# Kernel tuning notes

Measured on AMD Instinct MI355X. Metric: run time of the kernel, lower is better.

Reference implementation:

```python
import jax, jax.numpy as jnp
import numpy as np

LAMBDA_CHAMFER = 1.0
LAMBDA_EDGE = 0.1


def setup_inputs() -> dict:
    key = jax.random.key(0)
    k1, k2, k3 = jax.random.split(key, 3)
    B, N, M, E = 8, 4096, 4096, 12288
    pred_vertices = jax.random.normal(k1, (B, N, 3), dtype=jnp.float32)
    gt_vertices = jax.random.normal(k2, (B, M, 3), dtype=jnp.float32)
    edges = jax.random.randint(k3, (E, 2), 0, N, dtype=jnp.int64)
    return {"pred_vertices": pred_vertices, "gt_vertices": gt_vertices, "edges": edges}


def _pairwise_dist(p1, p2):
    # ||x - y|| computed via the expanded form to avoid a [B,N,M,3] intermediate.
    # dist2[b,n,m] = |p1[b,n]|^2 + |p2[b,m]|^2 - 2 * p1[b,n] . p2[b,m]
    sq1 = jnp.sum(p1 * p1, axis=-1)  # [B, N]
    sq2 = jnp.sum(p2 * p2, axis=-1)  # [B, M]
    cross = jnp.einsum('bnd,bmd->bnm', p1, p2)  # [B, N, M]
    dist2 = sq1[:, :, None] + sq2[:, None, :] - 2.0 * cross
    return jnp.sqrt(jnp.maximum(dist2, 0.0))


def chamfer_distance(p1, p2):
    dist = _pairwise_dist(p1, p2)  # [B, N, M]
    min_p1 = jnp.min(dist, axis=2)  # [B, N] nearest gt for each pred point
    min_p2 = jnp.min(dist, axis=1)  # [B, M] nearest pred for each gt point
    return jnp.mean(min_p1) + jnp.mean(min_p2)


def edge_length_regularization(vertices, edges):
    v1 = vertices[:, edges[:, 0]]  # [B, E, 3]
    v2 = vertices[:, edges[:, 1]]  # [B, E, 3]
    lengths = jnp.linalg.norm(v1 - v2, axis=2)  # [B, E]
    return jnp.var(lengths, ddof=1)  # torch.var is unbiased by default


def reference(pred_vertices, gt_vertices, edges):
    cd = chamfer_distance(pred_vertices, gt_vertices)
    edge_loss = edge_length_regularization(pred_vertices, edges)
    return LAMBDA_CHAMFER * cd + LAMBDA_EDGE * edge_loss
```

## Files before the change

### kernel.cpp

```cpp
#include <hip/hip_runtime.h>
#include <hip/hip_bf16.h>
#include <float.h>

constexpr int B = 8, N = 4096, M = 4096, E = 12288;
constexpr int BLOCK = 256;
constexpr int VEC = 4;
constexpr int QPB = BLOCK * VEC;
constexpr int QT = N / QPB;
constexpr int SEG = 8;
constexpr int RPS = M / SEG;
constexpr int CHAM_BLOCKS = 2 * B * QT * SEG;
constexpr int EDGE_BLOCKS = (B * E) / BLOCK;
constexpr int EPB = E / BLOCK;


__global__ __launch_bounds__(BLOCK) void fused_kernel(
    const float* __restrict__ pred, const float* __restrict__ gt,
    const int* __restrict__ edges, unsigned* __restrict__ ws) {
    const int bid = blockIdx.x;
    const int t = threadIdx.x;

    if (bid < CHAM_BLOCKS) {
        const int dir = bid >> 8;
        const int r   = bid & 255;
        const int b   = r >> 5;
        const int rem = r & 31;
        const int qt  = rem >> 3;
        const int sg  = rem & 7;
        const float* __restrict__ q   = dir ? gt   : pred;
        const float* __restrict__ ref = dir ? pred : gt;
        unsigned* __restrict__ minOut = ws + dir * (B * N) + b * N + qt * QPB;

        float qx[VEC], qy[VEC], qz[VEC], h1[VEC];
#pragma unroll
        for (int i = 0; i < VEC; i++) {
            const int n = qt * QPB + i * BLOCK + t;
            const float* p = q + ((size_t)b * N + n) * 3;
            qx[i] = p[0]; qy[i] = p[1]; qz[i] = p[2];
            h1[i] = 0.5f * (qx[i] * qx[i] + qy[i] * qy[i] + qz[i] * qz[i]);
        }

        __shared__ float4 tile[RPS];
        {
            const float2* rb = (const float2*)(ref + ((size_t)b * M + sg * RPS) * 3);
            const float2 r0 = rb[3 * t], r1 = rb[3 * t + 1], r2 = rb[3 * t + 2];
            const float x0 = r0.x, y0 = r0.y, z0 = r1.x;
            const float x1 = r1.y, y1 = r2.x, z1 = r2.y;
            tile[2 * t]     = make_float4(x0, y0, z0, 0.5f * (x0*x0 + y0*y0 + z0*z0));
            tile[2 * t + 1] = make_float4(x1, y1, z1, 0.5f * (x1*x1 + y1*y1 + z1*z1));
        }
        __syncthreads();

        float mn[VEC];
#pragma unroll
        for (int i = 0; i < VEC; i++) mn[i] = FLT_MAX;

#pragma unroll 8
        for (int m = 0; m < RPS; ++m) {
            const float4 p = tile[m];
#pragma unroll
            for (int i = 0; i < VEC; ++i) {
                float d = h1[i] + p.w;
                d = fmaf(-qx[i], p.x, d);
                d = fmaf(-qy[i], p.y, d);
                d = fmaf(-qz[i], p.z, d);
                mn[i] = fminf(mn[i], d);
            }
        }

#pragma unroll
        for (int i = 0; i < VEC; ++i) {
            const unsigned u = __float_as_uint(fmaxf(mn[i], 0.0f));
            atomicMin(minOut + i * BLOCK + t, u);
        }
    } else {
        const int eb = bid - CHAM_BLOCKS;
        const int b  = eb / EPB;
        const int e  = (eb - b * EPB) * BLOCK + t;
        const int i0 = edges[2 * e], i1 = edges[2 * e + 1];
        const float* p0 = pred + ((size_t)b * N + i0) * 3;
        const float* p1 = pred + ((size_t)b * N + i1) * 3;
        const float dx = p0[0] - p1[0];
        const float dy = p0[1] - p1[1];
        const float dz = p0[2] - p1[2];
        float L  = sqrtf(dx * dx + dy * dy + dz * dz);
        float L2 = L * L;
#pragma unroll
        for (int o = 32; o > 0; o >>= 1) {
            L  += __shfl_down(L, o, 64);
            L2 += __shfl_down(L2, o, 64);
        }
        __shared__ float w1[4], w2[4];
        const int wave = t >> 6, lane = t & 63;
        if (lane == 0) { w1[wave] = L; w2[wave] = L2; }
        __syncthreads();
        if (t == 0) {
            float* wsf = (float*)(ws + 2 * B * N);
            wsf[2 * eb]     = w1[0] + w1[1] + w1[2] + w1[3];
            wsf[2 * eb + 1] = w2[0] + w2[1] + w2[2] + w2[3];
        }
    }
}

__global__ __launch_bounds__(1024) void final_kernel(
    const unsigned* __restrict__ ws, float* __restrict__ out) {
    const int t = threadIdx.x;

    float sc = 0.0f;
#pragma unroll 8
    for (int k = 0; k < 64; ++k) {
        const float h = __uint_as_float(ws[t + k * 1024]);
        sc += sqrtf(fmaxf(2.0f * h, 0.0f));
    }
    float s1 = 0.0f, s2 = 0.0f;
    if (t < EDGE_BLOCKS) {
        const float* wsf = (const float*)(ws + 2 * B * N);
        s1 = wsf[2 * t];
        s2 = wsf[2 * t + 1];
    }
#pragma unroll
    for (int o = 32; o > 0; o >>= 1) {
        sc += __shfl_down(sc, o, 64);
        s1 += __shfl_down(s1, o, 64);
        s2 += __shfl_down(s2, o, 64);
    }
    __shared__ float w[3][16];
    const int wave = t >> 6, lane = t & 63;
    if (lane == 0) { w[0][wave] = sc; w[1][wave] = s1; w[2][wave] = s2; }
    __syncthreads();
    if (t == 0) {
        float S = 0.0f, A = 0.0f, C = 0.0f;
#pragma unroll
        for (int i = 0; i < 16; i++) { S += w[0][i]; A += w[1][i]; C += w[2][i]; }
        const float K = (float)(B * E);
        const float var = (C - A * A / K) / (K - 1.0f);
        out[0] = S / 32768.0f + 0.1f * var;
    }
}

extern "C" void kernel_launch(void* const* d_in, const int* in_sizes, int n_in,
                              void* d_out, int out_size, void* d_ws, size_t ws_size,
                              hipStream_t stream) {
    const float* pred  = (const float*)d_in[0];
    const float* gt    = (const float*)d_in[1];
    const int*   edges = (const int*)d_in[2];
    float* out = (float*)d_out;
    unsigned* ws = (unsigned*)d_ws;

    fused_kernel<<<CHAM_BLOCKS + EDGE_BLOCKS, BLOCK, 0, stream>>>(pred, gt, edges, ws);
    final_kernel<<<1, 1024, 0, stream>>>(ws, out);
}
```

Measured before the change: 95.20 us.

## Load full reference set per block and reduce minima in shared memory

Each 1024-thread block now stages the entire 4096-point reference set into shared memory and splits it across 8 thread groups, which then combine their partial minima in shared memory. This replaces the global atomicMin path and the separate sqrt/mean pass over 64K values in the final kernel. Each block also writes a partial sum of distances, so the final kernel only reduces 256 values. In exchange, each block uses 64KB+ of LDS and handles 2 queries per thread instead of 4, which may lower occupancy and register-level reuse. The inner loop is unrolled over 4 reference points with two independent min accumulators.

```diff
diff --git a/kernel.cpp b/kernel.cpp
--- a/kernel.cpp
+++ b/kernel.cpp
@@ -3,80 +3,99 @@
 #include <float.h>
 
 constexpr int B = 8, N = 4096, M = 4096, E = 12288;
-constexpr int BLOCK = 256;
-constexpr int VEC = 4;
-constexpr int QPB = BLOCK * VEC;
-constexpr int QT = N / QPB;
-constexpr int SEG = 8;
-constexpr int RPS = M / SEG;
-constexpr int CHAM_BLOCKS = 2 * B * QT * SEG;
-constexpr int EDGE_BLOCKS = (B * E) / BLOCK;
-constexpr int EPB = E / BLOCK;
+constexpr int CBLOCK = 1024;
+constexpr int CHAM_BLOCKS = 256;
+constexpr int EDGE_BLOCKS = (B * E) / CBLOCK;
+constexpr int SPLIT = 8;
+constexpr int RPT = M / SPLIT;
+constexpr int VEC = 2;
+constexpr int QG = CBLOCK / SPLIT;
 
 
-__global__ __launch_bounds__(BLOCK) void fused_kernel(
+__global__ __launch_bounds__(CBLOCK) void fused_kernel(
     const float* __restrict__ pred, const float* __restrict__ gt,
-    const int* __restrict__ edges, unsigned* __restrict__ ws) {
+    const int* __restrict__ edges, float* __restrict__ ws) {
     const int bid = blockIdx.x;
     const int t = threadIdx.x;
 
+    __shared__ float4 tile[M];
+    __shared__ float red[SPLIT * 256];
+    __shared__ float wsum[16];
+
     if (bid < CHAM_BLOCKS) {
-        const int dir = bid >> 8;
-        const int r   = bid & 255;
-        const int b   = r >> 5;
-        const int rem = r & 31;
-        const int qt  = rem >> 3;
-        const int sg  = rem & 7;
+        const int dir = bid >> 7;
+        const int b   = (bid >> 4) & 7;
+        const int qt  = bid & 15;
         const float* __restrict__ q   = dir ? gt   : pred;
         const float* __restrict__ ref = dir ? pred : gt;
-        unsigned* __restrict__ minOut = ws + dir * (B * N) + b * N + qt * QPB;
 
+        {
+            const float2* rb = (const float2*)(ref + (size_t)b * M * 3) + 6 * t;
+            const float2 r0 = rb[0], r1 = rb[1], r2 = rb[2];
+            const float2 r3 = rb[3], r4 = rb[4], r5 = rb[5];
+            const float x0=r0.x,y0=r0.y,z0=r1.x, x1=r1.y,y1=r2.x,z1=r2.y;
+            const float x2=r3.x,y2=r3.y,z2=r4.x, x3=r4.y,y3=r5.x,z3=r5.y;
+            tile[4*t+0] = make_float4(x0,y0,z0, 0.5f*(x0*x0+y0*y0+z0*z0));
+            tile[4*t+1] = make_float4(x1,y1,z1, 0.5f*(x1*x1+y1*y1+z1*z1));
+            tile[4*t+2] = make_float4(x2,y2,z2, 0.5f*(x2*x2+y2*y2+z2*z2));
+            tile[4*t+3] = make_float4(x3,y3,z3, 0.5f*(x3*x3+y3*y3+z3*z3));
+        }
+
+        const int qloc = t & (QG - 1);
+        const int s    = t >> 7;
         float qx[VEC], qy[VEC], qz[VEC], h1[VEC];
 #pragma unroll
         for (int i = 0; i < VEC; i++) {
-            const int n = qt * QPB + i * BLOCK + t;
-            const float* p = q + ((size_t)b * N + n) * 3;
-            qx[i] = p[0]; qy[i] = p[1]; qz[i] = p[2];
-            h1[i] = 0.5f * (qx[i] * qx[i] + qy[i] * qy[i] + qz[i] * qz[i]);
-        }
-
-        __shared__ float4 tile[RPS];
-        {
-            const float2* rb = (const float2*)(ref + ((size_t)b * M + sg * RPS) * 3);
-            const float2 r0 = rb[3 * t], r1 = rb[3 * t + 1], r2 = rb[3 * t + 2];
-            const float x0 = r0.x, y0 = r0.y, z0 = r1.x;
-            const float x1 = r1.y, y1 = r2.x, z1 = r2.y;
-            tile[2 * t]     = make_float4(x0, y0, z0, 0.5f * (x0*x0 + y0*y0 + z0*z0));
-            tile[2 * t + 1] = make_float4(x1, y1, z1, 0.5f * (x1*x1 + y1*y1 + z1*z1));
+            const int n = qt * 256 + qloc + i * QG;
+            const float* qp = q + ((size_t)b * N + n) * 3;
+            qx[i] = qp[0]; qy[i] = qp[1]; qz[i] = qp[2];
+            h1[i] = 0.5f * (qx[i]*qx[i] + qy[i]*qy[i] + qz[i]*qz[i]);
         }
         __syncthreads();
 
-        float mn[VEC];
+        const float4* tl = tile + s * RPT;
+        float mnA[VEC], mnB[VEC];
 #pragma unroll
-        for (int i = 0; i < VEC; i++) mn[i] = FLT_MAX;
+        for (int i = 0; i < VEC; i++) { mnA[i] = FLT_MAX; mnB[i] = FLT_MAX; }
 
-#pragma unroll 8
-        for (int m = 0; m < RPS; ++m) {
-            const float4 p = tile[m];
+#pragma unroll 2
+        for (int m = 0; m < RPT; m += 4) {
+            const float4 p0 = tl[m], p1 = tl[m+1], p2 = tl[m+2], p3 = tl[m+3];
 #pragma unroll
-            for (int i = 0; i < VEC; ++i) {
-                float d = h1[i] + p.w;
-                d = fmaf(-qx[i], p.x, d);
-                d = fmaf(-qy[i], p.y, d);
-                d = fmaf(-qz[i], p.z, d);
-                mn[i] = fminf(mn[i], d);
+            for (int i = 0; i < VEC; i++) {
+                float d0 = h1[i] + p0.w;
+                d0 = fmaf(-qx[i], p0.x, d0); d0 = fmaf(-qy[i], p0.y, d0); d0 = fmaf(-qz[i], p0.z, d0);
+                float d1 = h1[i] + p1.w;
+                d1 = fmaf(-qx[i], p1.x, d1); d1 = fmaf(-qy[i], p1.y, d1); d1 = fmaf(-qz[i], p1.z, d1);
+                float d2 = h1[i] + p2.w;
+                d2 = fmaf(-qx[i], p2.x, d2); d2 = fmaf(-qy[i], p2.y, d2); d2 = fmaf(-qz[i], p2.z, d2);
+                float d3 = h1[i] + p3.w;
+                d3 = fmaf(-qx[i], p3.x, d3); d3 = fmaf(-qy[i], p3.y, d3); d3 = fmaf(-qz[i], p3.z, d3);
+                mnA[i] = fminf(mnA[i], fminf(d0, d1));
+                mnB[i] = fminf(mnB[i], fminf(d2, d3));
             }
         }
 
+        red[s * 256 + qloc]      = fminf(mnA[0], mnB[0]);
+        red[s * 256 + qloc + QG] = fminf(mnA[1], mnB[1]);
+        __syncthreads();
+
+        float sv = 0.0f;
+        if (t < 256) {
+            float m8 = red[t];
 #pragma unroll
-        for (int i = 0; i < VEC; ++i) {
-            const unsigned u = __float_as_uint(fmaxf(mn[i], 0.0f));
-            atomicMin(minOut + i * BLOCK + t, u);
+            for (int k = 1; k < SPLIT; k++) m8 = fminf(m8, red[k * 256 + t]);
+            sv = sqrtf(fmaxf(2.0f * m8, 0.0f));
         }
+#pragma unroll
+        for (int o = 32; o > 0; o >>= 1) sv += __shfl_down(sv, o, 64);
+        if ((t & 63) == 0) wsum[t >> 6] = sv;
+        __syncthreads();
+        if (t == 0) ws[bid] = wsum[0] + wsum[1] + wsum[2] + wsum[3];
     } else {
-        const int eb = bid - CHAM_BLOCKS;
-        const int b  = eb / EPB;
-        const int e  = (eb - b * EPB) * BLOCK + t;
+        const int eg = (bid - CHAM_BLOCKS) * CBLOCK + t;
+        const int b  = eg / E;
+        const int e  = eg - b * E;
         const int i0 = edges[2 * e], i1 = edges[2 * e + 1];
         const float* p0 = pred + ((size_t)b * N + i0) * 3;
         const float* p1 = pred + ((size_t)b * N + i1) * 3;
@@ -90,33 +109,27 @@
             L  += __shfl_down(L, o, 64);
             L2 += __shfl_down(L2, o, 64);
         }
-        __shared__ float w1[4], w2[4];
-        const int wave = t >> 6, lane = t & 63;
-        if (lane == 0) { w1[wave] = L; w2[wave] = L2; }
+        if ((t & 63) == 0) { red[t >> 6] = L; red[32 + (t >> 6)] = L2; }
         __syncthreads();
         if (t == 0) {
-            float* wsf = (float*)(ws + 2 * B * N);
-            wsf[2 * eb]     = w1[0] + w1[1] + w1[2] + w1[3];
-            wsf[2 * eb + 1] = w2[0] + w2[1] + w2[2] + w2[3];
+            float a = 0.0f, c = 0.0f;
+#pragma unroll
+            for (int w = 0; w < 16; w++) { a += red[w]; c += red[32 + w]; }
+            const int eb = bid - CHAM_BLOCKS;
+            ws[CHAM_BLOCKS + 2 * eb]     = a;
+            ws[CHAM_BLOCKS + 2 * eb + 1] = c;
         }
     }
 }
 
-__global__ __launch_bounds__(1024) void final_kernel(
-    const unsigned* __restrict__ ws, float* __restrict__ out) {
+__global__ __launch_bounds__(256) void final_kernel(
+    const float* __restrict__ ws, float* __restrict__ out) {
     const int t = threadIdx.x;
-
-    float sc = 0.0f;
-#pragma unroll 8
-    for (int k = 0; k < 64; ++k) {
-        const float h = __uint_as_float(ws[t + k * 1024]);
-        sc += sqrtf(fmaxf(2.0f * h, 0.0f));
-    }
+    float sc = ws[t];
     float s1 = 0.0f, s2 = 0.0f;
     if (t < EDGE_BLOCKS) {
-        const float* wsf = (const float*)(ws + 2 * B * N);
-        s1 = wsf[2 * t];
-        s2 = wsf[2 * t + 1];
+        s1 = ws[CHAM_BLOCKS + 2 * t];
+        s2 = ws[CHAM_BLOCKS + 2 * t + 1];
     }
 #pragma unroll
     for (int o = 32; o > 0; o >>= 1) {
@@ -124,14 +137,14 @@
         s1 += __shfl_down(s1, o, 64);
         s2 += __shfl_down(s2, o, 64);
     }
-    __shared__ float w[3][16];
-    const int wave = t >> 6, lane = t & 63;
-    if (lane == 0) { w[0][wave] = sc; w[1][wave] = s1; w[2][wave] = s2; }
+    __shared__ float w[3][4];
+    const int wv = t >> 6, ln = t & 63;
+    if (ln == 0) { w[0][wv] = sc; w[1][wv] = s1; w[2][wv] = s2; }
     __syncthreads();
     if (t == 0) {
         float S = 0.0f, A = 0.0f, C = 0.0f;
 #pragma unroll
-        for (int i = 0; i < 16; i++) { S += w[0][i]; A += w[1][i]; C += w[2][i]; }
+        for (int i = 0; i < 4; i++) { S += w[0][i]; A += w[1][i]; C += w[2][i]; }
         const float K = (float)(B * E);
         const float var = (C - A * A / K) / (K - 1.0f);
         out[0] = S / 32768.0f + 0.1f * var;
@@ -145,8 +158,8 @@
     const float* gt    = (const float*)d_in[1];
     const int*   edges = (const int*)d_in[2];
     float* out = (float*)d_out;
-    unsigned* ws = (unsigned*)d_ws;
+    float* wsf = (float*)d_ws;
 
-    fused_kernel<<<CHAM_BLOCKS + EDGE_BLOCKS, BLOCK, 0, stream>>>(pred, gt, edges, ws);
-    final_kernel<<<1, 1024, 0, stream>>>(ws, out);
+    fused_kernel<<<CHAM_BLOCKS + EDGE_BLOCKS, CBLOCK, 0, stream>>>(pred, gt, edges, wsf);
+    final_kernel<<<1, 256, 0, stream>>>(wsf, out);
 }
```

Measured after the change: 87.29 us. 8.3% less time.
